# Performance work log

Measured on AMD Instinct MI355X. Metric: run time of the kernel, lower is better.

Reference implementation:

```python
import jax, jax.numpy as jnp
import numpy as np

SHADOW_OFFSET = -1000.0
EPS_SIGMA = 1e-05
SIGMA_DIV = 2.1


def setup_inputs() -> dict:
    key = jax.random.key(0)
    k1, k2, k3, k4, k5, k6 = jax.random.split(key, 6)
    B, N, M, K, Kp, Din, Dout = 2, 65536, 16384, 32, 15, 64, 128
    points_xyz = jax.random.normal(k1, (B, N, 3), dtype=jnp.float32)
    features = jax.random.normal(k2, (B, Din, N), dtype=jnp.float32)
    center_xyz = jax.random.normal(k3, (B, M, 3), dtype=jnp.float32)
    neighbor_indices = jax.random.randint(k4, (B, M, K), 0, N + 1, dtype=jnp.int64)
    # kernel points in unit ball, 'center' fixed at origin (stand-in for load_kernels)
    kp = jax.random.normal(k5, (Kp, 3), dtype=jnp.float32)
    kp = kp / (jnp.linalg.norm(kp, axis=-1, keepdims=True) + 1e-6) * jax.random.uniform(k6, (Kp, 1)) ** (1.0 / 3.0)
    kernel_points = kp.at[0].set(0.0)
    # kaiming_uniform(a=sqrt(5)) on [Kp, Din, Dout]: fan_in = Din*Dout per torch semantics
    fan_in = Din * Dout
    bound = jnp.sqrt(6.0 / ((1.0 + 5.0) * fan_in)) * jnp.sqrt(3.0) / jnp.sqrt(3.0)
    bound = float(np.sqrt(6.0 / (6.0 * fan_in)))
    weights = jax.random.uniform(jax.random.fold_in(key, 7), (Kp, Din, Dout), minval=-bound, maxval=bound, dtype=jnp.float32)
    return {"points_xyz": points_xyz, "features": features, "center_xyz": center_xyz,
            "neighbor_indices": neighbor_indices, "kernel_points": kernel_points, "weights": weights}


def reference(points_xyz, features, center_xyz, neighbor_indices, kernel_points, weights):
    B, N, _ = points_xyz.shape
    M, K = neighbor_indices.shape[1], neighbor_indices.shape[2]
    Din = features.shape[1]
    # [B,N,3+Din] point coords + features, plus shadow point at index N
    points = jnp.concatenate([points_xyz, jnp.swapaxes(features, 1, 2)], axis=-1)
    shadow = jnp.zeros((B, 1, 3 + Din), points.dtype).at[:, :, :3].set(SHADOW_OFFSET)
    points = jnp.concatenate([points, shadow], axis=1)  # [B,N+1,3+Din]
    idx = neighbor_indices.reshape(B, M * K)
    gathered = jnp.take_along_axis(points, idx[:, :, None], axis=1).reshape(B, M, K, 3 + Din)
    neighbors_xyz = gathered[..., :3] - center_xyz[:, :, None, :]   # [B,M,K,3]
    neighbors_feats = gathered[..., 3:]                              # [B,M,K,Din]
    dist = jnp.sqrt(jnp.sum(neighbors_xyz ** 2, axis=3))             # [B,M,K]
    m_dist = jnp.max(dist, axis=2, keepdims=True)                    # [B,M,1]
    # radius=None path: kernel points scaled per center by max neighbor distance
    kp = kernel_points[None, None, :, :] * m_dist[:, :, :, None]     # [B,M,Kp,3]
    diffs = neighbors_xyz[:, :, :, None, :] - kp[:, :, None, :, :]   # [B,M,K,Kp,3]
    sq_d = jnp.sum(diffs ** 2, axis=4)                               # [B,M,K,Kp]
    sigma = m_dist[..., None] / SIGMA_DIV + EPS_SIGMA                # [B,M,1,1]
    w = jnp.clip(1.0 - jnp.sqrt(sq_d) / sigma, 0.0)                  # [B,M,K,Kp]
    weighted = jnp.einsum('bmkp,bmkd->bmpd', w, neighbors_feats)     # [B,M,Kp,Din]
    out = jnp.einsum('bmpd,pdo->bmo', weighted, weights)             # [B,M,Dout]
    return jnp.swapaxes(out, 1, 2)                                   # [B,Dout,M]
```

## Files before the change

kernel.cpp:

```cpp
#include <hip/hip_runtime.h>
#include <hip/hip_bf16.h>
#include <stdint.h>

#define B_    2
#define N_    65536
#define M_    16384
#define K_    32
#define KP_   15
#define DIN_  64
#define DOUT_ 128

typedef __bf16 bf16x8 __attribute__((ext_vector_type(8)));
typedef float  f32x4  __attribute__((ext_vector_type(4)));
typedef float  f32x2  __attribute__((ext_vector_type(2)));

__device__ inline unsigned short f2bf(float f) {
    union { float f; unsigned int i; } v; v.f = f;
    unsigned int x = v.i;
    return (unsigned short)((x + 0x7fffu + ((x >> 16) & 1u)) >> 16);
}

__global__ __launch_bounds__(256) void transpose_feats(const float* __restrict__ feats,
                                                       unsigned short* __restrict__ featT) {
    const int b  = blockIdx.y;
    const int n0 = blockIdx.x * 64;
    const int t  = threadIdx.x;
    if (n0 >= N_) {
        if (t < 32)
            ((unsigned int*)(featT + ((size_t)b * (N_ + 1) + N_) * DIN_))[t] = 0u;
        return;
    }
    __shared__ float tile[64][65];
    const int nl = t & 63, dl = t >> 6;
    #pragma unroll
    for (int i = 0; i < 16; ++i) {
        int d = dl + 4 * i;
        tile[d][nl] = feats[((size_t)b * DIN_ + d) * N_ + n0 + nl];
    }
    __syncthreads();
    const int d2 = (t & 31) * 2;
    const int nr = t >> 5;
    #pragma unroll
    for (int i = 0; i < 8; ++i) {
        int n = nr + 8 * i;
        unsigned int u = ((unsigned int)f2bf(tile[d2 + 1][n]) << 16) | f2bf(tile[d2][n]);
        ((unsigned int*)(featT + ((size_t)b * (N_ + 1) + n0 + n) * DIN_))[t & 31] = u;
    }
}

__global__ __launch_bounds__(256) void build_wt(const float* __restrict__ w,
                                                unsigned short* __restrict__ wt) {
    int tid = blockIdx.x * 256 + threadIdx.x;
    if (tid < 960 * 128) {
        int pd = tid >> 7, o = tid & 127;
        wt[o * 960 + pd] = f2bf(w[tid]);
    }
}

__global__ __launch_bounds__(256, 3) void gather_weight(
    const float* __restrict__ points_xyz,
    const float* __restrict__ center_xyz,
    const int*   __restrict__ nidx,
    const float* __restrict__ kpts,
    const unsigned short* __restrict__ featT,
    unsigned short* __restrict__ weighted) {

    __shared__ __align__(16) float        wlds[8 * KP_ * 32];
    __shared__ __align__(16) unsigned int fbuf[8 * 32 * 32];

    const int t  = threadIdx.x;
    const int b  = blockIdx.y;
    const int m0 = blockIdx.x * 8;
    const size_t ibase = ((size_t)b * M_ + m0) * K_;

    uint4 v[8];
    const int part = t & 7, rbase = t >> 3;
    #pragma unroll
    for (int i = 0; i < 8; ++i) {
        int r = i * 32 + rbase;
        int n = nidx[ibase + r];
        v[i] = *(const uint4*)(featT + ((size_t)b * (N_ + 1) + n) * DIN_ + part * 8);
    }

    {
        const int m = t >> 5, k = t & 31;
        int n = nidx[ibase + t];
        float px, py, pz;
        if (n < N_) {
            const float* p = points_xyz + ((size_t)b * N_ + n) * 3;
            px = p[0]; py = p[1]; pz = p[2];
        } else {
            px = py = pz = -1000.0f;
        }
        const float* c = center_xyz + ((size_t)b * M_ + m0 + m) * 3;
        float dx = px - c[0], dy = py - c[1], dz = pz - c[2];
        float md = __builtin_amdgcn_sqrtf(dx * dx + dy * dy + dz * dz);
        #pragma unroll
        for (int s = 16; s > 0; s >>= 1)
            md = fmaxf(md, __shfl_xor(md, s));
        float rsig = __builtin_amdgcn_rcpf(md * (1.0f / 2.1f) + 1e-5f);
        #pragma unroll
        for (int p = 0; p < KP_; ++p) {
            float ex = dx - kpts[p * 3 + 0] * md;
            float ey = dy - kpts[p * 3 + 1] * md;
            float ez = dz - kpts[p * 3 + 2] * md;
            float wv = 1.0f - __builtin_amdgcn_sqrtf(ex * ex + ey * ey + ez * ez) * rsig;
            wlds[(m * KP_ + p) * 32 + k] = wv > 0.0f ? wv : 0.0f;
        }
    }

    #pragma unroll
    for (int i = 0; i < 8; ++i)
        ((uint4*)fbuf)[(i * 32 + rbase) * 8 + part] = v[i];
    __syncthreads();

    const int m = t >> 5, d2 = t & 31;
    f32x2 acc[KP_];
    #pragma unroll
    for (int p = 0; p < KP_; ++p) acc[p] = (f32x2){0.f, 0.f};

    const unsigned int* fcol = &fbuf[(m * 32) * 32 + d2];
    const float* wbase = &wlds[m * KP_ * 32];

    #pragma unroll
    for (int k4 = 0; k4 < 8; ++k4) {
        f32x2 fv[4];
        #pragma unroll
        for (int j = 0; j < 4; ++j) {
            unsigned int u = fcol[(k4 * 4 + j) * 32];
            union { unsigned int i; float f; } lo, hi;
            lo.i = u << 16; hi.i = u & 0xffff0000u;
            fv[j] = (f32x2){lo.f, hi.f};
        }
        #pragma unroll
        for (int p = 0; p < KP_; ++p) {
            float4 w4 = *(const float4*)(wbase + p * 32 + k4 * 4);
            acc[p] += fv[0] * w4.x;
            acc[p] += fv[1] * w4.y;
            acc[p] += fv[2] * w4.z;
            acc[p] += fv[3] * w4.w;
        }
    }

    unsigned int* wout = (unsigned int*)weighted + (size_t)(b * M_ + m0 + m) * 480 + d2;
    #pragma unroll
    for (int p = 0; p < KP_; ++p) {
        unsigned int u = ((unsigned int)f2bf(acc[p][1]) << 16) | f2bf(acc[p][0]);
        wout[p * 32] = u;
    }
}

#define GLOAD_LDS16(g, l) __builtin_amdgcn_global_load_lds( \
    (const __attribute__((address_space(1))) unsigned int*)(g), \
    (__attribute__((address_space(3))) unsigned int*)(l), 16, 0, 0)

__global__ __launch_bounds__(512, 2) void gemm_out(
    const unsigned short* __restrict__ weightedG,
    const unsigned short* __restrict__ wtG,
    float* __restrict__ out) {

    __shared__ __align__(16) char smem[65536];

    const int t = threadIdx.x;
    const int w = t >> 6, lane = t & 63;
    const int bm0 = blockIdx.x * 128;
    const int b = bm0 >> 14, m_in_b = bm0 & (M_ - 1);

    const int wr = w >> 2, wc = w & 3;
    const int wm = wr * 64, wo = wc * 32;

    f32x4 acc[4][2] = {};

    auto stage = [&](int buf, int kt) {
        #pragma unroll
        for (int i = 0; i < 2; ++i) {
            int chunk = w * 2 + i;
            int L = chunk * 1024 + lane * 16;
            int row = L >> 7, col = L & 127;
            int scol = col ^ ((row & 7) << 4);
            const char* src = (const char*)weightedG + (size_t)(bm0 + row) * 1920 + kt * 128 + scol;
            GLOAD_LDS16(src, smem + buf * 16384 + chunk * 1024);
        }
        #pragma unroll
        for (int i = 0; i < 2; ++i) {
            int chunk = w * 2 + i;
            int L = chunk * 1024 + lane * 16;
            int row = L >> 7, col = L & 127;
            int scol = col ^ ((row & 7) << 4);
            const char* src = (const char*)wtG + (size_t)row * 1920 + kt * 128 + scol;
            GLOAD_LDS16(src, smem + 32768 + buf * 16384 + chunk * 1024);
        }
    };

    stage(0, 0);
    __syncthreads();

    for (int kt = 0; kt < 15; ++kt) {
        int cur = kt & 1;
        if (kt < 14) stage(cur ^ 1, kt + 1);
        const char* lA = smem + cur * 16384;
        const char* lB = smem + 32768 + cur * 16384;
        #pragma unroll
        for (int ks = 0; ks < 2; ++ks) {
            bf16x8 af[4], bfr[2];
            const int kcol = ks * 64 + (lane >> 4) * 16;
            #pragma unroll
            for (int mf = 0; mf < 4; ++mf) {
                int row = wm + mf * 16 + (lane & 15);
                af[mf] = *(const bf16x8*)(lA + row * 128 + (kcol ^ ((row & 7) << 4)));
            }
            #pragma unroll
            for (int of = 0; of < 2; ++of) {
                int row = wo + of * 16 + (lane & 15);
                bfr[of] = *(const bf16x8*)(lB + row * 128 + (kcol ^ ((row & 7) << 4)));
            }
            #pragma unroll
            for (int mf = 0; mf < 4; ++mf)
                #pragma unroll
                for (int of = 0; of < 2; ++of)
                    acc[mf][of] = __builtin_amdgcn_mfma_f32_16x16x32_bf16(
                        af[mf], bfr[of], acc[mf][of], 0, 0, 0);
        }
        __syncthreads();
    }

    #pragma unroll
    for (int mf = 0; mf < 4; ++mf)
        #pragma unroll
        for (int of = 0; of < 2; ++of) {
            int o  = wo + of * 16 + (lane & 15);
            int mr = wm + mf * 16 + (lane >> 4) * 4;
            int byte = (o * 512 + mr * 4) ^ ((o & 7) << 4);
            *(f32x4*)(smem + byte) = acc[mf][of];
        }
    __syncthreads();
    #pragma unroll
    for (int pass = 0; pass < 4; ++pass) {
        int o  = pass * 32 + (t >> 4);
        int mc = (t & 15) * 8;
        int b0 = (o * 512 + mc * 4)       ^ ((o & 7) << 4);
        int b1 = (o * 512 + (mc + 4) * 4) ^ ((o & 7) << 4);
        f32x4 v0 = *(const f32x4*)(smem + b0);
        f32x4 v1 = *(const f32x4*)(smem + b1);
        float* dst = out + ((size_t)(b * DOUT_ + o)) * M_ + m_in_b + mc;
        *(f32x4*)dst = v0;
        *(f32x4*)(dst + 4) = v1;
    }
}

extern "C" void kernel_launch(void* const* d_in, const int* in_sizes, int n_in,
                              void* d_out, int out_size, void* d_ws, size_t ws_size,
                              hipStream_t stream) {
    const float* points_xyz = (const float*)d_in[0];
    const float* features   = (const float*)d_in[1];
    const float* center_xyz = (const float*)d_in[2];
    const int*   nidx       = (const int*)d_in[3];
    const float* kpts       = (const float*)d_in[4];
    const float* weights    = (const float*)d_in[5];
    float* out = (float*)d_out;

    unsigned short* featT    = (unsigned short*)d_ws;
    unsigned short* wt       = (unsigned short*)((char*)d_ws + 16777472);
    unsigned short* weighted = (unsigned short*)((char*)d_ws + 17023232);

    transpose_feats<<<dim3((N_ + 64) / 64, B_), 256, 0, stream>>>(features, featT);
    build_wt<<<480, 256, 0, stream>>>(weights, wt);
    gather_weight<<<dim3(M_ / 8, B_), 256, 0, stream>>>(points_xyz, center_xyz, nidx,
                                                        kpts, featT, weighted);
    gemm_out<<<B_ * M_ / 128, 512, 0, stream>>>(weighted, wt, out);
}
```

Baseline: 154.0 us.

## Fuse gather-weighting and output GEMM into one kernel with prepacked MFMA weight fragments

Merges the gather/kernel-point weighting kernel and the separate bf16 GEMM into a single kernel. Each block now handles 16 centers with 512 threads, keeps the weighted features in LDS, and runs MFMA directly against weight fragments that a new build kernel prepacks in register-fragment order. This removes the round trip of the intermediate weighted tensor through global memory and one kernel launch. The cost is that each block streams the full weight matrix from global/L2 for only 16 rows, with occupancy limited to one block per CU and stores of only 16 contiguous floats per output row.

```diff
diff --git a/kernel.cpp b/kernel.cpp
--- a/kernel.cpp
+++ b/kernel.cpp
@@ -9,6 +9,8 @@
 #define KP_   15
 #define DIN_  64
 #define DOUT_ 128
+#define TM    16
+#define WPITCH 968
 
 typedef __bf16 bf16x8 __attribute__((ext_vector_type(8)));
 typedef float  f32x4  __attribute__((ext_vector_type(4)));
@@ -48,36 +50,47 @@
     }
 }
 
-__global__ __launch_bounds__(256) void build_wt(const float* __restrict__ w,
-                                                unsigned short* __restrict__ wt) {
-    int tid = blockIdx.x * 256 + threadIdx.x;
-    if (tid < 960 * 128) {
-        int pd = tid >> 7, o = tid & 127;
-        wt[o * 960 + pd] = f2bf(w[tid]);
-    }
-}
-
-__global__ __launch_bounds__(256, 3) void gather_weight(
+__global__ __launch_bounds__(256) void build_wtfrag(const float* __restrict__ w,
+                                                    unsigned short* __restrict__ wf) {
+    int q = blockIdx.x * 256 + threadIdx.x;
+    if (q >= 15360) return;
+    int otile = q / 1920, r = q % 1920;
+    int ks = r >> 6, lane = r & 63;
+    int o  = otile * 16 + (lane & 15);
+    int kb = ks * 32 + (lane >> 4) * 8;
+    unsigned int d[4];
+    #pragma unroll
+    for (int j = 0; j < 4; ++j) {
+        unsigned short lo = f2bf(w[(size_t)(kb + 2 * j) * 128 + o]);
+        unsigned short hi = f2bf(w[(size_t)(kb + 2 * j + 1) * 128 + o]);
+        d[j] = ((unsigned int)hi << 16) | lo;
+    }
+    *(uint4*)(wf + (size_t)q * 8) = make_uint4(d[0], d[1], d[2], d[3]);
+}
+
+__global__ __launch_bounds__(512, 1) void kpconv_fused(
     const float* __restrict__ points_xyz,
     const float* __restrict__ center_xyz,
     const int*   __restrict__ nidx,
     const float* __restrict__ kpts,
     const unsigned short* __restrict__ featT,
-    unsigned short* __restrict__ weighted) {
-
-    __shared__ __align__(16) float        wlds[8 * KP_ * 32];
-    __shared__ __align__(16) unsigned int fbuf[8 * 32 * 32];
+    const unsigned short* __restrict__ wtFrag,
+    float* __restrict__ out) {
+
+    __shared__ __align__(16) unsigned int  fbuf[TM * 32 * 32];
+    __shared__ __align__(16) float         wlds[TM * KP_ * 32];
+    __shared__ __align__(16) unsigned short wgt[TM * WPITCH];
 
     const int t  = threadIdx.x;
     const int b  = blockIdx.y;
-    const int m0 = blockIdx.x * 8;
+    const int m0 = blockIdx.x * TM;
     const size_t ibase = ((size_t)b * M_ + m0) * K_;
 
     uint4 v[8];
     const int part = t & 7, rbase = t >> 3;
     #pragma unroll
     for (int i = 0; i < 8; ++i) {
-        int r = i * 32 + rbase;
+        int r = i * 64 + rbase;
         int n = nidx[ibase + r];
         v[i] = *(const uint4*)(featT + ((size_t)b * (N_ + 1) + n) * DIN_ + part * 8);
     }
@@ -111,140 +124,80 @@
 
     #pragma unroll
     for (int i = 0; i < 8; ++i)
-        ((uint4*)fbuf)[(i * 32 + rbase) * 8 + part] = v[i];
+        ((uint4*)fbuf)[(i * 64 + rbase) * 8 + part] = v[i];
     __syncthreads();
 
-    const int m = t >> 5, d2 = t & 31;
-    f32x2 acc[KP_];
-    #pragma unroll
-    for (int p = 0; p < KP_; ++p) acc[p] = (f32x2){0.f, 0.f};
-
-    const unsigned int* fcol = &fbuf[(m * 32) * 32 + d2];
-    const float* wbase = &wlds[m * KP_ * 32];
-
-    #pragma unroll
-    for (int k4 = 0; k4 < 8; ++k4) {
-        f32x2 fv[4];
-        #pragma unroll
-        for (int j = 0; j < 4; ++j) {
-            unsigned int u = fcol[(k4 * 4 + j) * 32];
-            union { unsigned int i; float f; } lo, hi;
-            lo.i = u << 16; hi.i = u & 0xffff0000u;
-            fv[j] = (f32x2){lo.f, hi.f};
-        }
-        #pragma unroll
-        for (int p = 0; p < KP_; ++p) {
-            float4 w4 = *(const float4*)(wbase + p * 32 + k4 * 4);
-            acc[p] += fv[0] * w4.x;
-            acc[p] += fv[1] * w4.y;
-            acc[p] += fv[2] * w4.z;
-            acc[p] += fv[3] * w4.w;
-        }
-    }
-
-    unsigned int* wout = (unsigned int*)weighted + (size_t)(b * M_ + m0 + m) * 480 + d2;
-    #pragma unroll
-    for (int p = 0; p < KP_; ++p) {
-        unsigned int u = ((unsigned int)f2bf(acc[p][1]) << 16) | f2bf(acc[p][0]);
-        wout[p * 32] = u;
-    }
-}
-
-#define GLOAD_LDS16(g, l) __builtin_amdgcn_global_load_lds( \
-    (const __attribute__((address_space(1))) unsigned int*)(g), \
-    (__attribute__((address_space(3))) unsigned int*)(l), 16, 0, 0)
-
-__global__ __launch_bounds__(512, 2) void gemm_out(
-    const unsigned short* __restrict__ weightedG,
-    const unsigned short* __restrict__ wtG,
-    float* __restrict__ out) {
-
-    __shared__ __align__(16) char smem[65536];
-
-    const int t = threadIdx.x;
-    const int w = t >> 6, lane = t & 63;
-    const int bm0 = blockIdx.x * 128;
-    const int b = bm0 >> 14, m_in_b = bm0 & (M_ - 1);
-
-    const int wr = w >> 2, wc = w & 3;
-    const int wm = wr * 64, wo = wc * 32;
-
-    f32x4 acc[4][2] = {};
-
-    auto stage = [&](int buf, int kt) {
-        #pragma unroll
-        for (int i = 0; i < 2; ++i) {
-            int chunk = w * 2 + i;
-            int L = chunk * 1024 + lane * 16;
-            int row = L >> 7, col = L & 127;
-            int scol = col ^ ((row & 7) << 4);
-            const char* src = (const char*)weightedG + (size_t)(bm0 + row) * 1920 + kt * 128 + scol;
-            GLOAD_LDS16(src, smem + buf * 16384 + chunk * 1024);
-        }
-        #pragma unroll
-        for (int i = 0; i < 2; ++i) {
-            int chunk = w * 2 + i;
-            int L = chunk * 1024 + lane * 16;
-            int row = L >> 7, col = L & 127;
-            int scol = col ^ ((row & 7) << 4);
-            const char* src = (const char*)wtG + (size_t)row * 1920 + kt * 128 + scol;
-            GLOAD_LDS16(src, smem + 32768 + buf * 16384 + chunk * 1024);
-        }
-    };
-
-    stage(0, 0);
-    __syncthreads();
-
-    for (int kt = 0; kt < 15; ++kt) {
-        int cur = kt & 1;
-        if (kt < 14) stage(cur ^ 1, kt + 1);
-        const char* lA = smem + cur * 16384;
-        const char* lB = smem + 32768 + cur * 16384;
-        #pragma unroll
-        for (int ks = 0; ks < 2; ++ks) {
-            bf16x8 af[4], bfr[2];
-            const int kcol = ks * 64 + (lane >> 4) * 16;
+    {
+        const int m = t >> 5, d2 = t & 31;
+        f32x2 acc[KP_];
+        #pragma unroll
+        for (int p = 0; p < KP_; ++p) acc[p] = (f32x2){0.f, 0.f};
+
+        const unsigned int* fcol = &fbuf[(m * 32) * 32 + d2];
+        const float* wbase = &wlds[m * KP_ * 32];
+
+        #pragma unroll
+        for (int k4 = 0; k4 < 8; ++k4) {
+            f32x2 fv[4];
             #pragma unroll
-            for (int mf = 0; mf < 4; ++mf) {
-                int row = wm + mf * 16 + (lane & 15);
-                af[mf] = *(const bf16x8*)(lA + row * 128 + (kcol ^ ((row & 7) << 4)));
+            for (int j = 0; j < 4; ++j) {
+                unsigned int u = fcol[(k4 * 4 + j) * 32];
+                union { unsigned int i; float f; } lo, hi;
+                lo.i = u << 16; hi.i = u & 0xffff0000u;
+                fv[j] = (f32x2){lo.f, hi.f};
             }
             #pragma unroll
-            for (int of = 0; of < 2; ++of) {
-                int row = wo + of * 16 + (lane & 15);
-                bfr[of] = *(const bf16x8*)(lB + row * 128 + (kcol ^ ((row & 7) << 4)));
+            for (int p = 0; p < KP_; ++p) {
+                float4 w4 = *(const float4*)(wbase + p * 32 + k4 * 4);
+                acc[p] += fv[0] * w4.x;
+                acc[p] += fv[1] * w4.y;
+                acc[p] += fv[2] * w4.z;
+                acc[p] += fv[3] * w4.w;
             }
-            #pragma unroll
-            for (int mf = 0; mf < 4; ++mf)
-                #pragma unroll
-                for (int of = 0; of < 2; ++of)
-                    acc[mf][of] = __builtin_amdgcn_mfma_f32_16x16x32_bf16(
-                        af[mf], bfr[of], acc[mf][of], 0, 0, 0);
-        }
-        __syncthreads();
-    }
-
-    #pragma unroll
-    for (int mf = 0; mf < 4; ++mf)
-        #pragma unroll
-        for (int of = 0; of < 2; ++of) {
-            int o  = wo + of * 16 + (lane & 15);
-            int mr = wm + mf * 16 + (lane >> 4) * 4;
-            int byte = (o * 512 + mr * 4) ^ ((o & 7) << 4);
-            *(f32x4*)(smem + byte) = acc[mf][of];
-        }
+        }
+
+        unsigned int* wrow = (unsigned int*)wgt;
+        #pragma unroll
+        for (int p = 0; p < KP_; ++p) {
+            unsigned int u = ((unsigned int)f2bf(acc[p][1]) << 16) | f2bf(acc[p][0]);
+            wrow[m * (WPITCH / 2) + p * 32 + d2] = u;
+        }
+    }
     __syncthreads();
-    #pragma unroll
-    for (int pass = 0; pass < 4; ++pass) {
-        int o  = pass * 32 + (t >> 4);
-        int mc = (t & 15) * 8;
-        int b0 = (o * 512 + mc * 4)       ^ ((o & 7) << 4);
-        int b1 = (o * 512 + (mc + 4) * 4) ^ ((o & 7) << 4);
-        f32x4 v0 = *(const f32x4*)(smem + b0);
-        f32x4 v1 = *(const f32x4*)(smem + b1);
-        float* dst = out + ((size_t)(b * DOUT_ + o)) * M_ + m_in_b + mc;
-        *(f32x4*)dst = v0;
-        *(f32x4*)(dst + 4) = v1;
+
+    {
+        const int w = t >> 6, lane = t & 63;
+        const char* aBase = (const char*)wgt + (lane & 15) * (WPITCH * 2) + (lane >> 4) * 16;
+        const unsigned short* bPtr = wtFrag + ((size_t)(w * 30) * 64 + lane) * 8;
+
+        f32x4 dacc = {0.f, 0.f, 0.f, 0.f};
+        bf16x8 b0 = *(const bf16x8*)(bPtr);
+        bf16x8 b1 = *(const bf16x8*)(bPtr + 512);
+        bf16x8 b2 = *(const bf16x8*)(bPtr + 1024);
+        bf16x8 b3 = *(const bf16x8*)(bPtr + 1536);
+        bf16x8 b4 = *(const bf16x8*)(bPtr + 2048);
+
+        #define S2_STEP(BX, KS, LD)                                           \
+            {                                                                 \
+                bf16x8 a = *(const bf16x8*)(aBase + (KS) * 64);               \
+                dacc = __builtin_amdgcn_mfma_f32_16x16x32_bf16(a, BX, dacc,   \
+                                                               0, 0, 0);      \
+                if ((LD) < 30) BX = *(const bf16x8*)(bPtr + (size_t)(LD) * 512); \
+            }
+
+        for (int mi = 0; mi < 6; ++mi) {
+            int ks = mi * 5;
+            S2_STEP(b0, ks + 0, ks + 5);
+            S2_STEP(b1, ks + 1, ks + 6);
+            S2_STEP(b2, ks + 2, ks + 7);
+            S2_STEP(b3, ks + 3, ks + 8);
+            S2_STEP(b4, ks + 4, ks + 9);
+        }
+        #undef S2_STEP
+
+        const int o = w * 16 + (lane & 15);
+        float* dst = out + ((size_t)b * DOUT_ + o) * M_ + m0 + (lane >> 4) * 4;
+        *(f32x4*)dst = dacc;
     }
 }
 
@@ -259,13 +212,11 @@
     const float* weights    = (const float*)d_in[5];
     float* out = (float*)d_out;
 
-    unsigned short* featT    = (unsigned short*)d_ws;
-    unsigned short* wt       = (unsigned short*)((char*)d_ws + 16777472);
-    unsigned short* weighted = (unsigned short*)((char*)d_ws + 17023232);
+    unsigned short* featT  = (unsigned short*)d_ws;
+    unsigned short* wtFrag = (unsigned short*)((char*)d_ws + 16777472);
 
     transpose_feats<<<dim3((N_ + 64) / 64, B_), 256, 0, stream>>>(features, featT);
-    build_wt<<<480, 256, 0, stream>>>(weights, wt);
-    gather_weight<<<dim3(M_ / 8, B_), 256, 0, stream>>>(points_xyz, center_xyz, nidx,
-                                                        kpts, featT, weighted);
-    gemm_out<<<B_ * M_ / 128, 512, 0, stream>>>(weighted, wt, out);
-}
+    build_wtfrag<<<60, 256, 0, stream>>>(weights, wtFrag);
+    kpconv_fused<<<dim3(M_ / TM, B_), 512, 0, stream>>>(points_xyz, center_xyz, nidx,
+                                                        kpts, featT, wtFrag, out);
+}
```

New measurement: 170.7 us. 1.11x slower.
